# Performance work log

Measured on AMD Instinct MI355X. Metric: run time of the kernel, lower is better.

The kernel has to match this reference:

```python
import jax, jax.numpy as jnp
import numpy as np

N_NEIGHBORS = 3


def square_distance(src, dst):
    # src: [B,N,3], dst: [B,M,3] -> [B,N,M]
    d = -2.0 * jnp.einsum('bnc,bmc->bnm', src, dst)
    d = d + jnp.sum(src * src, axis=-1)[:, :, None]
    d = d + jnp.sum(dst * dst, axis=-1)[:, None, :]
    return d


def setup_inputs() -> dict:
    key = jax.random.key(0)
    k1, k2, k3 = jax.random.split(key, 3)
    B, N_q, N_k, C = 4, 8192, 2048, 128
    xyz_q = jax.random.normal(k1, (B, N_q, 3), dtype=jnp.float32)
    xyz_k = jax.random.normal(k2, (B, N_k, 3), dtype=jnp.float32)
    v_k = jax.random.normal(k3, (B, N_k, C), dtype=jnp.float32)
    return {"xyz_q": xyz_q, "xyz_k": xyz_k, "v_k": v_k}


def reference(xyz_q, xyz_k, v_k):
    # pairwise squared distances [B,N_q,N_k]
    sqrdists = square_distance(xyz_q, xyz_k)
    # kNN: smallest nsample distances per query
    neg_dist, idx = jax.lax.top_k(-sqrdists, N_NEIGHBORS)  # [B,N_q,k]
    dist_nearest = jnp.take_along_axis(sqrdists, idx, axis=2)
    dist_nearest = jnp.maximum(dist_nearest, 1e-10)
    weights = 1.0 / dist_nearest
    weights = weights / jnp.sum(weights, axis=-1, keepdims=True)
    # gather neighbor features: [B,N_q,k,C]
    grouped_v = jax.vmap(lambda v, i: v[i])(v_k, idx)
    # inverse-distance-weighted interpolation
    v_q = jnp.einsum('bnk,bnkc->bnc', weights, grouped_v)
    return v_q
```

## Files before the change

kernel.cpp:

```cpp
#include <hip/hip_runtime.h>
#include <cfloat>

#define BB 4
#define NQ 8192
#define NK 2048
#define CC 128
#define C4 (CC / 4)

#define QPB 64
#define SPLITS 16
#define KPS (NK / SPLITS)
#define NTHR (QPB * SPLITS)

__global__ __launch_bounds__(NTHR, 8) void fp_fused(
    const float*  __restrict__ xyz_q,
    const float*  __restrict__ xyz_k,
    const float4* __restrict__ vk,
    float4*       __restrict__ out)
{
    __shared__ float4 ks[NK];
    __shared__ unsigned long long rd[NTHR][4];
    __shared__ float sw[QPB][4];
    __shared__ int   si[QPB][4];

    const int b     = blockIdx.y;
    const int qbase = blockIdx.x * QPB;
    const int tid   = threadIdx.x;
    const int lane  = tid & 63;
    const int split = tid >> 6;
    const int q     = qbase + lane;

    {
        const float* kb = xyz_k + (size_t)b * NK * 3;
        #pragma unroll
        for (int i = tid; i < NK; i += NTHR) {
            ks[i] = make_float4(kb[i * 3 + 0], kb[i * 3 + 1], kb[i * 3 + 2], 0.0f);
        }
    }

    const float qx = xyz_q[(b * NQ + q) * 3 + 0];
    const float qy = xyz_q[(b * NQ + q) * 3 + 1];
    const float qz = xyz_q[(b * NQ + q) * 3 + 2];

    __syncthreads();

    const int kbeg = __builtin_amdgcn_readfirstlane(split * KPS);

    float u0 = FLT_MAX, u1 = FLT_MAX, u2 = FLT_MAX, u3 = FLT_MAX;

    #pragma unroll 8
    for (int j = 0; j < KPS; ++j) {
        float4 kk = ks[kbeg + j];
        float dx = qx - kk.x, dy = qy - kk.y, dz = qz - kk.z;
        float t = fmaf(dx, dx, fmaf(dy, dy, dz * dz));
        float p = __uint_as_float((__float_as_uint(t) & 0xFFFFFF80u) | (unsigned)j);
        u3 = __builtin_amdgcn_fmed3f(p, u2, u3);
        u2 = __builtin_amdgcn_fmed3f(p, u1, u2);
        u1 = __builtin_amdgcn_fmed3f(p, u0, u1);
        u0 = fminf(u0, p);
    }

    {
        float uu[4] = { u0, u1, u2, u3 };
        #pragma unroll
        for (int c = 0; c < 4; ++c) {
            int kidx = kbeg + (int)(__float_as_uint(uu[c]) & 0x7Fu);
            float4 ka = ks[kidx];
            double dx = (double)qx - (double)ka.x;
            double dy = (double)qy - (double)ka.y;
            double dz = (double)qz - (double)ka.z;
            double dd = dx * dx + dy * dy + dz * dz;
            unsigned long long pk =
                (((unsigned long long)__double_as_longlong(dd)) & ~0x7FFull)
                | (unsigned long long)kidx;
            rd[tid][c] = pk;
        }
    }
    __syncthreads();

    if (tid < QPB) {
        double m0 = DBL_MAX, m1 = DBL_MAX, m2 = DBL_MAX;
        #pragma unroll 4
        for (int s = 0; s < SPLITS; ++s) {
            #pragma unroll
            for (int c = 0; c < 4; ++c) {
                double x = __longlong_as_double((long long)rd[s * QPB + lane][c]);
                double a1 = fmax(x, m1), a0 = fmax(x, m0);
                m2 = fmin(m2, a1);
                m1 = fmin(m1, a0);
                m0 = fmin(m0, x);
            }
        }
        unsigned long long b0 = (unsigned long long)__double_as_longlong(m0);
        unsigned long long b1 = (unsigned long long)__double_as_longlong(m1);
        unsigned long long b2 = (unsigned long long)__double_as_longlong(m2);
        double e0 = __longlong_as_double((long long)(b0 & ~0x7FFull));
        double e1 = __longlong_as_double((long long)(b1 & ~0x7FFull));
        double e2 = __longlong_as_double((long long)(b2 & ~0x7FFull));
        e0 = fmax(e0, 1e-10);
        e1 = fmax(e1, 1e-10);
        e2 = fmax(e2, 1e-10);
        double w0 = 1.0 / e0, w1 = 1.0 / e1, w2 = 1.0 / e2;
        double s  = w0 + w1 + w2;
        sw[lane][0] = (float)(w0 / s);
        sw[lane][1] = (float)(w1 / s);
        sw[lane][2] = (float)(w2 / s);
        si[lane][0] = (int)(b0 & 0x7FFull);
        si[lane][1] = (int)(b1 & 0x7FFull);
        si[lane][2] = (int)(b2 & 0x7FFull);
    }
    __syncthreads();

    const float4* vb = vk + (size_t)b * NK * C4;
    float4* ob = out + ((size_t)b * NQ + qbase) * C4;
    #pragma unroll
    for (int r = 0; r < (QPB * C4) / NTHR; ++r) {
        int o  = r * NTHR + tid;
        int qq = o >> 5;
        int c4 = o & (C4 - 1);
        float w0 = sw[qq][0], w1 = sw[qq][1], w2 = sw[qq][2];
        int   j0 = si[qq][0], j1 = si[qq][1], j2 = si[qq][2];
        float4 v0 = vb[j0 * C4 + c4];
        float4 v1 = vb[j1 * C4 + c4];
        float4 v2 = vb[j2 * C4 + c4];
        float4 res;
        res.x = fmaf(w0, v0.x, fmaf(w1, v1.x, w2 * v2.x));
        res.y = fmaf(w0, v0.y, fmaf(w1, v1.y, w2 * v2.y));
        res.z = fmaf(w0, v0.z, fmaf(w1, v1.z, w2 * v2.z));
        res.w = fmaf(w0, v0.w, fmaf(w1, v1.w, w2 * v2.w));
        ob[o] = res;
    }
}

extern "C" void kernel_launch(void* const* d_in, const int* in_sizes, int n_in,
                              void* d_out, int out_size, void* d_ws, size_t ws_size,
                              hipStream_t stream)
{
    const float* xyz_q = (const float*)d_in[0];
    const float* xyz_k = (const float*)d_in[1];
    const float* v_k   = (const float*)d_in[2];

    fp_fused<<<dim3(NQ / QPB, BB), dim3(NTHR), 0, stream>>>(
        xyz_q, xyz_k, (const float4*)v_k, (float4*)d_out);
}
```

Measured before the change: 88.88 us.

## Process two queries per thread to reuse key loads from LDS

Each thread now scores two queries against the same key slice, doubling queries per block to 128 while keeping 1024 threads. Every LDS key load now serves two distance computations, halving LDS traffic per query and also halving the per-block key staging cost. The partial-result buffer is transposed to [split][c][query] so the merge stage reads consecutive lanes without bank conflicts. The cost is more registers per thread and half as many blocks, with occupancy hints lowered to four blocks per CU.

```diff
diff --git a/kernel.cpp b/kernel.cpp
--- a/kernel.cpp
+++ b/kernel.cpp
@@ -7,19 +7,19 @@
 #define CC 128
 #define C4 (CC / 4)
 
-#define QPB 64
+#define QPB 128
 #define SPLITS 16
 #define KPS (NK / SPLITS)
-#define NTHR (QPB * SPLITS)
+#define NTHR 1024
 
-__global__ __launch_bounds__(NTHR, 8) void fp_fused(
+__global__ __launch_bounds__(NTHR, 4) void fp_fused(
     const float*  __restrict__ xyz_q,
     const float*  __restrict__ xyz_k,
     const float4* __restrict__ vk,
     float4*       __restrict__ out)
 {
     __shared__ float4 ks[NK];
-    __shared__ unsigned long long rd[NTHR][4];
+    __shared__ unsigned long long rd[SPLITS][4][QPB];
     __shared__ float sw[QPB][4];
     __shared__ int   si[QPB][4];
 
@@ -28,7 +28,6 @@
     const int tid   = threadIdx.x;
     const int lane  = tid & 63;
     const int split = tid >> 6;
-    const int q     = qbase + lane;
 
     {
         const float* kb = xyz_k + (size_t)b * NK * 3;
@@ -38,42 +37,72 @@
         }
     }
 
-    const float qx = xyz_q[(b * NQ + q) * 3 + 0];
-    const float qy = xyz_q[(b * NQ + q) * 3 + 1];
-    const float qz = xyz_q[(b * NQ + q) * 3 + 2];
+    const int q0 = qbase + lane;
+    const int q1 = q0 + 64;
+    const float ax = xyz_q[(b * NQ + q0) * 3 + 0];
+    const float ay = xyz_q[(b * NQ + q0) * 3 + 1];
+    const float az = xyz_q[(b * NQ + q0) * 3 + 2];
+    const float bx = xyz_q[(b * NQ + q1) * 3 + 0];
+    const float by = xyz_q[(b * NQ + q1) * 3 + 1];
+    const float bz = xyz_q[(b * NQ + q1) * 3 + 2];
 
     __syncthreads();
 
     const int kbeg = __builtin_amdgcn_readfirstlane(split * KPS);
 
-    float u0 = FLT_MAX, u1 = FLT_MAX, u2 = FLT_MAX, u3 = FLT_MAX;
+    float a0 = FLT_MAX, a1 = FLT_MAX, a2 = FLT_MAX, a3 = FLT_MAX;
+    float c0 = FLT_MAX, c1 = FLT_MAX, c2 = FLT_MAX, c3 = FLT_MAX;
 
     #pragma unroll 8
     for (int j = 0; j < KPS; ++j) {
         float4 kk = ks[kbeg + j];
-        float dx = qx - kk.x, dy = qy - kk.y, dz = qz - kk.z;
-        float t = fmaf(dx, dx, fmaf(dy, dy, dz * dz));
-        float p = __uint_as_float((__float_as_uint(t) & 0xFFFFFF80u) | (unsigned)j);
-        u3 = __builtin_amdgcn_fmed3f(p, u2, u3);
-        u2 = __builtin_amdgcn_fmed3f(p, u1, u2);
-        u1 = __builtin_amdgcn_fmed3f(p, u0, u1);
-        u0 = fminf(u0, p);
+        {
+            float dx = ax - kk.x, dy = ay - kk.y, dz = az - kk.z;
+            float t = fmaf(dx, dx, fmaf(dy, dy, dz * dz));
+            float p = __uint_as_float((__float_as_uint(t) & 0xFFFFFF80u) | (unsigned)j);
+            a3 = __builtin_amdgcn_fmed3f(p, a2, a3);
+            a2 = __builtin_amdgcn_fmed3f(p, a1, a2);
+            a1 = __builtin_amdgcn_fmed3f(p, a0, a1);
+            a0 = fminf(a0, p);
+        }
+        {
+            float dx = bx - kk.x, dy = by - kk.y, dz = bz - kk.z;
+            float t = fmaf(dx, dx, fmaf(dy, dy, dz * dz));
+            float p = __uint_as_float((__float_as_uint(t) & 0xFFFFFF80u) | (unsigned)j);
+            c3 = __builtin_amdgcn_fmed3f(p, c2, c3);
+            c2 = __builtin_amdgcn_fmed3f(p, c1, c2);
+            c1 = __builtin_amdgcn_fmed3f(p, c0, c1);
+            c0 = fminf(c0, p);
+        }
     }
 
     {
-        float uu[4] = { u0, u1, u2, u3 };
+        float ua[4] = { a0, a1, a2, a3 };
+        float ub[4] = { c0, c1, c2, c3 };
         #pragma unroll
         for (int c = 0; c < 4; ++c) {
-            int kidx = kbeg + (int)(__float_as_uint(uu[c]) & 0x7Fu);
-            float4 ka = ks[kidx];
-            double dx = (double)qx - (double)ka.x;
-            double dy = (double)qy - (double)ka.y;
-            double dz = (double)qz - (double)ka.z;
-            double dd = dx * dx + dy * dy + dz * dz;
-            unsigned long long pk =
-                (((unsigned long long)__double_as_longlong(dd)) & ~0x7FFull)
-                | (unsigned long long)kidx;
-            rd[tid][c] = pk;
+            {
+                int kidx = kbeg + (int)(__float_as_uint(ua[c]) & 0x7Fu);
+                float4 ka = ks[kidx];
+                double dx = (double)ax - (double)ka.x;
+                double dy = (double)ay - (double)ka.y;
+                double dz = (double)az - (double)ka.z;
+                double dd = dx * dx + dy * dy + dz * dz;
+                rd[split][c][lane] =
+                    (((unsigned long long)__double_as_longlong(dd)) & ~0x7FFull)
+                    | (unsigned long long)kidx;
+            }
+            {
+                int kidx = kbeg + (int)(__float_as_uint(ub[c]) & 0x7Fu);
+                float4 ka = ks[kidx];
+                double dx = (double)bx - (double)ka.x;
+                double dy = (double)by - (double)ka.y;
+                double dz = (double)bz - (double)ka.z;
+                double dd = dx * dx + dy * dy + dz * dz;
+                rd[split][c][lane + 64] =
+                    (((unsigned long long)__double_as_longlong(dd)) & ~0x7FFull)
+                    | (unsigned long long)kidx;
+            }
         }
     }
     __syncthreads();
@@ -84,10 +113,10 @@
         for (int s = 0; s < SPLITS; ++s) {
             #pragma unroll
             for (int c = 0; c < 4; ++c) {
-                double x = __longlong_as_double((long long)rd[s * QPB + lane][c]);
-                double a1 = fmax(x, m1), a0 = fmax(x, m0);
-                m2 = fmin(m2, a1);
-                m1 = fmin(m1, a0);
+                double x = __longlong_as_double((long long)rd[s][c][tid]);
+                double t1 = fmax(x, m1), t0 = fmax(x, m0);
+                m2 = fmin(m2, t1);
+                m1 = fmin(m1, t0);
                 m0 = fmin(m0, x);
             }
         }
@@ -102,12 +131,12 @@
         e2 = fmax(e2, 1e-10);
         double w0 = 1.0 / e0, w1 = 1.0 / e1, w2 = 1.0 / e2;
         double s  = w0 + w1 + w2;
-        sw[lane][0] = (float)(w0 / s);
-        sw[lane][1] = (float)(w1 / s);
-        sw[lane][2] = (float)(w2 / s);
-        si[lane][0] = (int)(b0 & 0x7FFull);
-        si[lane][1] = (int)(b1 & 0x7FFull);
-        si[lane][2] = (int)(b2 & 0x7FFull);
+        sw[tid][0] = (float)(w0 / s);
+        sw[tid][1] = (float)(w1 / s);
+        sw[tid][2] = (float)(w2 / s);
+        si[tid][0] = (int)(b0 & 0x7FFull);
+        si[tid][1] = (int)(b1 & 0x7FFull);
+        si[tid][2] = (int)(b2 & 0x7FFull);
     }
     __syncthreads();
 
```

New measurement: 91.43 us. +2.9%, slower.

## Use expanded-norm distances and defer fp64 refinement to merged top-4

Applied to the files above, without the earlier changes.

The inner distance loop now uses the expanded form |k|^2 - 2 q·k + |q|^2, with key norms precomputed into the w slot of the shared key array, so each candidate costs three FMAs plus an add. Per-split candidates are stored as packed 32-bit floats in a transposed shared layout instead of fp64 recomputed per split. The merge keeps a global top-4, and only those four get exact fp64 distances and a sorting network, which removes 64 fp64 distance computations per query. The cost is that the expanded form can lose precision through cancellation, so keeping four candidates is meant to absorb ordering errors among the true top-3.

```diff
diff --git a/kernel.cpp b/kernel.cpp
--- a/kernel.cpp
+++ b/kernel.cpp
@@ -19,7 +19,7 @@
     float4*       __restrict__ out)
 {
     __shared__ float4 ks[NK];
-    __shared__ unsigned long long rd[NTHR][4];
+    __shared__ unsigned rd[SPLITS][4][QPB];
     __shared__ float sw[QPB][4];
     __shared__ int   si[QPB][4];
 
@@ -34,13 +34,16 @@
         const float* kb = xyz_k + (size_t)b * NK * 3;
         #pragma unroll
         for (int i = tid; i < NK; i += NTHR) {
-            ks[i] = make_float4(kb[i * 3 + 0], kb[i * 3 + 1], kb[i * 3 + 2], 0.0f);
+            float x = kb[i * 3 + 0], y = kb[i * 3 + 1], z = kb[i * 3 + 2];
+            ks[i] = make_float4(x, y, z, fmaf(x, x, fmaf(y, y, z * z)));
         }
     }
 
     const float qx = xyz_q[(b * NQ + q) * 3 + 0];
     const float qy = xyz_q[(b * NQ + q) * 3 + 1];
     const float qz = xyz_q[(b * NQ + q) * 3 + 2];
+    const float m2x = -2.0f * qx, m2y = -2.0f * qy, m2z = -2.0f * qz;
+    const float qq2 = fmaf(qx, qx, fmaf(qy, qy, qz * qz));
 
     __syncthreads();
 
@@ -51,8 +54,9 @@
     #pragma unroll 8
     for (int j = 0; j < KPS; ++j) {
         float4 kk = ks[kbeg + j];
-        float dx = qx - kk.x, dy = qy - kk.y, dz = qz - kk.z;
-        float t = fmaf(dx, dx, fmaf(dy, dy, dz * dz));
+        float t = fmaf(kk.x, m2x,
+                  fmaf(kk.y, m2y,
+                  fmaf(kk.z, m2z, kk.w + qq2)));
         float p = __uint_as_float((__float_as_uint(t) & 0xFFFFFF80u) | (unsigned)j);
         u3 = __builtin_amdgcn_fmed3f(p, u2, u3);
         u2 = __builtin_amdgcn_fmed3f(p, u1, u2);
@@ -60,54 +64,80 @@
         u0 = fminf(u0, p);
     }
 
-    {
-        float uu[4] = { u0, u1, u2, u3 };
-        #pragma unroll
-        for (int c = 0; c < 4; ++c) {
-            int kidx = kbeg + (int)(__float_as_uint(uu[c]) & 0x7Fu);
-            float4 ka = ks[kidx];
-            double dx = (double)qx - (double)ka.x;
-            double dy = (double)qy - (double)ka.y;
-            double dz = (double)qz - (double)ka.z;
-            double dd = dx * dx + dy * dy + dz * dz;
-            unsigned long long pk =
-                (((unsigned long long)__double_as_longlong(dd)) & ~0x7FFull)
-                | (unsigned long long)kidx;
-            rd[tid][c] = pk;
-        }
-    }
+    rd[split][0][lane] = __float_as_uint(u0);
+    rd[split][1][lane] = __float_as_uint(u1);
+    rd[split][2][lane] = __float_as_uint(u2);
+    rd[split][3][lane] = __float_as_uint(u3);
     __syncthreads();
 
     if (tid < QPB) {
-        double m0 = DBL_MAX, m1 = DBL_MAX, m2 = DBL_MAX;
+        double m0 = DBL_MAX, m1 = DBL_MAX, m2 = DBL_MAX, m3 = DBL_MAX;
         #pragma unroll 4
         for (int s = 0; s < SPLITS; ++s) {
             #pragma unroll
             for (int c = 0; c < 4; ++c) {
-                double x = __longlong_as_double((long long)rd[s * QPB + lane][c]);
-                double a1 = fmax(x, m1), a0 = fmax(x, m0);
-                m2 = fmin(m2, a1);
-                m1 = fmin(m1, a0);
+                unsigned pb = rd[s][c][tid];
+                float vf = __uint_as_float(pb & 0xFFFFFF80u);
+                unsigned long long gidx =
+                    (unsigned long long)(s * KPS) + (pb & 0x7Fu);
+                unsigned long long xb =
+                    (unsigned long long)__double_as_longlong((double)vf) | gidx;
+                double x = __longlong_as_double((long long)xb);
+                m3 = fmin(m3, fmax(x, m2));
+                m2 = fmin(m2, fmax(x, m1));
+                m1 = fmin(m1, fmax(x, m0));
                 m0 = fmin(m0, x);
             }
         }
-        unsigned long long b0 = (unsigned long long)__double_as_longlong(m0);
-        unsigned long long b1 = (unsigned long long)__double_as_longlong(m1);
-        unsigned long long b2 = (unsigned long long)__double_as_longlong(m2);
-        double e0 = __longlong_as_double((long long)(b0 & ~0x7FFull));
-        double e1 = __longlong_as_double((long long)(b1 & ~0x7FFull));
-        double e2 = __longlong_as_double((long long)(b2 & ~0x7FFull));
-        e0 = fmax(e0, 1e-10);
-        e1 = fmax(e1, 1e-10);
-        e2 = fmax(e2, 1e-10);
+
+        double d0, d1, d2, d3;
+        int    i0, i1, i2, i3;
+        {
+            unsigned long long mb[4] = {
+                (unsigned long long)__double_as_longlong(m0),
+                (unsigned long long)__double_as_longlong(m1),
+                (unsigned long long)__double_as_longlong(m2),
+                (unsigned long long)__double_as_longlong(m3)
+            };
+            double dd[4]; int ii[4];
+            #pragma unroll
+            for (int c = 0; c < 4; ++c) {
+                int kidx = (int)(mb[c] & 0x7FFull);
+                float4 ka = ks[kidx];
+                double dx = (double)qx - (double)ka.x;
+                double dy = (double)qy - (double)ka.y;
+                double dz = (double)qz - (double)ka.z;
+                dd[c] = dx * dx + dy * dy + dz * dz;
+                ii[c] = kidx;
+            }
+            d0 = dd[0]; d1 = dd[1]; d2 = dd[2]; d3 = dd[3];
+            i0 = ii[0]; i1 = ii[1]; i2 = ii[2]; i3 = ii[3];
+        }
+
+        #define CSW(da, db, ia, ib)                                     \
+            { bool c_ = (da) > (db);                                    \
+              double dt_ = c_ ? (db) : (da); (db) = c_ ? (da) : (db);   \
+              (da) = dt_;                                               \
+              int it_ = c_ ? (ib) : (ia); (ib) = c_ ? (ia) : (ib);      \
+              (ia) = it_; }
+        CSW(d0, d1, i0, i1);
+        CSW(d2, d3, i2, i3);
+        CSW(d0, d2, i0, i2);
+        CSW(d1, d3, i1, i3);
+        CSW(d1, d2, i1, i2);
+        #undef CSW
+
+        double e0 = fmax(d0, 1e-10);
+        double e1 = fmax(d1, 1e-10);
+        double e2 = fmax(d2, 1e-10);
         double w0 = 1.0 / e0, w1 = 1.0 / e1, w2 = 1.0 / e2;
         double s  = w0 + w1 + w2;
-        sw[lane][0] = (float)(w0 / s);
-        sw[lane][1] = (float)(w1 / s);
-        sw[lane][2] = (float)(w2 / s);
-        si[lane][0] = (int)(b0 & 0x7FFull);
-        si[lane][1] = (int)(b1 & 0x7FFull);
-        si[lane][2] = (int)(b2 & 0x7FFull);
+        sw[tid][0] = (float)(w0 / s);
+        sw[tid][1] = (float)(w1 / s);
+        sw[tid][2] = (float)(w2 / s);
+        si[tid][0] = i0;
+        si[tid][1] = i1;
+        si[tid][2] = i2;
     }
     __syncthreads();
 
```

New measurement: 88.34 us. No clear change (-0.6%).
